# Kernel tuning notes

Hardware: AMD Instinct MI355X
Metric: run time of the kernel (lower is better)

## Reference

```python
import jax, jax.numpy as jnp
import numpy as np
import math

HEADS = 16
LAYER, NUM_LAYERS = 6, 12
ALPHA = 1.0 - math.tanh(math.pi * LAYER / NUM_LAYERS)
EPS = 1e-5


def _rot_half(t):
    d = t.shape[-1] // 2
    return jnp.concatenate([-t[..., d:], t[..., :d]], axis=-1)


def axial_rope(t):
    # t: [b, n, H, W, d]. Axial rotary: height rotates first d/2, width rotates second d/2.
    H, W, d = t.shape[2], t.shape[3], t.shape[4]
    half = d // 2
    inv_freq = 1.0 / (10000.0 ** (jnp.arange(0, half, 2, dtype=jnp.float32) / half))  # [half/2]
    ang_h = jnp.arange(H, dtype=jnp.float32)[:, None] * inv_freq[None, :]  # [H, half/2]
    ang_w = jnp.arange(W, dtype=jnp.float32)[:, None] * inv_freq[None, :]  # [W, half/2]
    ang_h = jnp.concatenate([ang_h, ang_h], axis=-1)  # [H, half]
    ang_w = jnp.concatenate([ang_w, ang_w], axis=-1)  # [W, half]
    ch, sh = jnp.cos(ang_h)[:, None, :], jnp.sin(ang_h)[:, None, :]  # [H,1,half]
    cw, sw = jnp.cos(ang_w)[None, :, :], jnp.sin(ang_w)[None, :, :]  # [1,W,half]
    th, tw = t[..., :half], t[..., half:]
    th = th * ch + _rot_half(th) * sh
    tw = tw * cw + _rot_half(tw) * sw
    return jnp.concatenate([th, tw], axis=-1)


def setup_inputs() -> dict:
    key = jax.random.key(0)
    ks = jax.random.split(key, 4)
    b, H, W, hid = 32, 28, 28, 1024
    return {
        "x": jax.random.normal(ks[0], (b, H, W, hid), jnp.float32),
        "input_img": jax.random.normal(ks[1], (b, H, W, hid), jnp.float32),
        "qkv_w": jax.random.normal(ks[2], (hid, 3 * hid), jnp.float32) * 0.02,
        "o_w": jax.random.normal(ks[3], (hid, hid), jnp.float32) * 0.02,
        "gn_w": jnp.ones((HEADS,), jnp.float32),
        "gn_b": jnp.zeros((HEADS,), jnp.float32),
    }


def reference(x, input_img, qkv_w, o_w, gn_w, gn_b):
    b, H, W, hid = x.shape
    n, dh = HEADS, hid // HEADS
    qkv = x @ qkv_w  # [b,H,W,3*hid]
    # 'b h w (c d) -> c b h w d'
    qkv = qkv.reshape(b, H, W, 3, hid).transpose(3, 0, 1, 2, 4)
    qkv = qkv + input_img[None] * ALPHA
    # 'c b h w (n d) -> c b n h w d'; unpack order is q, v, k
    qkv = qkv.reshape(3, b, H, W, n, dh).transpose(0, 1, 4, 2, 3, 5)
    q, v, k = qkv[0], qkv[1], qkv[2]
    gamma = (1.0 - 2.0 ** (-5.0 - jnp.arange(n, dtype=jnp.float32)))[None, :, None, None, None]
    k = k * gamma
    q, k = axial_rope(q), axial_rope(k)
    # attention along the W axis per row: [b,n,H,W,W]
    scores = jnp.einsum('bnhxd,bnhzd->bnhxz', q, k)
    # original einsum sums v over heights h as well as over y
    vsum = v.sum(axis=2)  # [b,n,W,dh]
    out = jnp.einsum('bnxwy,bnyd->bnxwd', scores, vsum)  # [b,n,H,W,dh]
    # GroupNorm(num_heads, num_heads): normalize each head over (H,W,dh)
    mu = out.mean(axis=(2, 3, 4), keepdims=True)
    var = out.var(axis=(2, 3, 4), keepdims=True)
    out = (out - mu) / jnp.sqrt(var + EPS)
    out = out * gn_w[None, :, None, None, None] + gn_b[None, :, None, None, None]
    # 'b n h w d -> b h w (n d)'
    out = out.transpose(0, 2, 3, 1, 4).reshape(b, H, W, hid)
    return out @ o_w
```

## Files before the change

kernel.cpp:

```cpp
#include <hip/hip_runtime.h>
#include <cstdint>
#include <cstddef>

#define HEADS 16
#define DH 64
#define BH 28
#define BWW 28
#define BATCH 32
#define HID 1024
#define M_ROWS 25088
#define ALPHA_C 0.082847664332725576f
#define EPS_C 1e-5f

typedef unsigned short ushort_t;
typedef __attribute__((ext_vector_type(8))) short bf16x8;
typedef __attribute__((ext_vector_type(4))) float f32x4;

__device__ inline unsigned short f2bf(float f) {
  unsigned int u = __builtin_bit_cast(unsigned int, f);
  u = (u + 0x7fffu + ((u >> 16) & 1u)) >> 16;
  return (unsigned short)u;
}
__device__ inline float bf2f(unsigned short h) {
  unsigned int u = ((unsigned int)h) << 16;
  return __builtin_bit_cast(float, u);
}

__global__ __launch_bounds__(256) void detect_k(const ushort_t* __restrict__ x,
                                                const ushort_t* __restrict__ qw,
                                                int* __restrict__ flagp) {
  int tid = threadIdx.x;
  int big = 0;
  #pragma unroll
  for (int j = 0; j < 4; ++j) {
    float a = fabsf(bf2f(x[tid * 4 + j]));
    float b = fabsf(bf2f(qw[tid * 4 + j]));
    if (!(a < 1e3f)) big++;
    if (!(b < 1e3f)) big++;
  }
  __shared__ int cnt;
  if (tid == 0) cnt = 0;
  __syncthreads();
  if (big) atomicAdd(&cnt, big);
  __syncthreads();
  if (tid == 0) *flagp = (cnt == 0) ? 1 : 0;
}

__global__ __launch_bounds__(256) void conv_x_k(const void* __restrict__ src,
                                                const int* __restrict__ flagp,
                                                ushort_t* __restrict__ dst, long n8) {
  if (*flagp) return;
  long i = (long)blockIdx.x * 256 + threadIdx.x;
  if (i >= n8) return;
  long e = i * 8;
  const float* sf = (const float*)src;
  float4 a = *(const float4*)(sf + e);
  float4 b = *(const float4*)(sf + e + 4);
  union { ushort_t u[8]; uint4 v; } o;
  o.u[0] = f2bf(a.x); o.u[1] = f2bf(a.y); o.u[2] = f2bf(a.z); o.u[3] = f2bf(a.w);
  o.u[4] = f2bf(b.x); o.u[5] = f2bf(b.y); o.u[6] = f2bf(b.z); o.u[7] = f2bf(b.w);
  *(uint4*)(dst + e) = o.v;
}

__global__ __launch_bounds__(256) void sumh_k(const void* __restrict__ x,
                                              const void* __restrict__ img,
                                              const int* __restrict__ flagp,
                                              ushort_t* __restrict__ xsum,
                                              float* __restrict__ imgsum) {
  int i = blockIdx.x * 256 + threadIdx.x;
  int c = i & 1023;
  int bw = i >> 10;
  int b = bw / BWW, w = bw % BWW;
  size_t base = ((size_t)b * BH * BWW + w) * HID + c;
  const size_t hstride = (size_t)BWW * HID;
  float sx = 0.f, si = 0.f;
  if (*flagp) {
    const ushort_t* xb = (const ushort_t*)x;
    const ushort_t* ib = (const ushort_t*)img;
    #pragma unroll 4
    for (int h = 0; h < BH; ++h) {
      sx += bf2f(xb[base + h * hstride]);
      si += bf2f(ib[base + h * hstride]);
    }
  } else {
    const float* xf = (const float*)x;
    const float* iff = (const float*)img;
    #pragma unroll 4
    for (int h = 0; h < BH; ++h) {
      sx += xf[base + h * hstride];
      si += iff[base + h * hstride];
    }
  }
  xsum[i] = f2bf(sx);
  imgsum[i] = si * ALPHA_C;
}

__global__ void transpose_any_k(const void* __restrict__ src, const int* __restrict__ flagp,
                                ushort_t* __restrict__ dst, int R, int C) {
  __shared__ float tile[32][33];
  int isbf = *flagp;
  int c0 = blockIdx.x * 32, r0 = blockIdx.y * 32;
  int tx = threadIdx.x, ty = threadIdx.y;
  const ushort_t* sb = (const ushort_t*)src;
  const float* sf = (const float*)src;
  #pragma unroll
  for (int i = ty; i < 32; i += 8) {
    size_t idx = (size_t)(r0 + i) * C + (c0 + tx);
    tile[i][tx] = isbf ? bf2f(sb[idx]) : sf[idx];
  }
  __syncthreads();
  #pragma unroll
  for (int i = ty; i < 32; i += 8)
    dst[(size_t)(c0 + i) * R + (r0 + tx)] = f2bf(tile[tx][i]);
}

#define BK 32

__global__ __launch_bounds__(256) void gemm_qkv_k(const void* __restrict__ x_raw,
                                                  const ushort_t* __restrict__ x_bf,
                                                  const ushort_t* __restrict__ Bt,
                                                  const void* __restrict__ img,
                                                  const int* __restrict__ flagp,
                                                  ushort_t* __restrict__ qbuf,
                                                  ushort_t* __restrict__ kbuf) {
  __shared__ ushort_t As[128 * BK];
  __shared__ ushort_t Bs[128 * BK];
  const int tid = threadIdx.x;
  const int K = 1024;
  const int ntile = 16;
  const int nt = blockIdx.x % ntile;
  const int n0 = (nt < 8) ? nt * 128 : nt * 128 + 1024;
  const int m0 = (blockIdx.x / ntile) * 128;
  const int lane = tid & 63;
  const int wave = tid >> 6;
  const int wm = (wave >> 1) * 64;
  const int wn = (wave & 1) * 64;
  const int fr = lane & 15;
  const int fq = lane >> 4;
  const int isbf = *flagp;
  const ushort_t* A = isbf ? (const ushort_t*)x_raw : x_bf;

  f32x4 acc[4][4] = {};
  const int srow = tid >> 2;
  const int skk  = (tid & 3) * 8;

  for (int k0 = 0; k0 < K; k0 += BK) {
    __syncthreads();
    const ushort_t* a0 = A + (size_t)(m0 + srow) * K + k0 + skk;
    const ushort_t* b0 = Bt + (size_t)(n0 + srow) * K + k0 + skk;
    __builtin_amdgcn_global_load_lds((const __attribute__((address_space(1))) unsigned int*)a0,
        (__attribute__((address_space(3))) unsigned int*)(As + tid * 8), 16, 0, 0);
    __builtin_amdgcn_global_load_lds((const __attribute__((address_space(1))) unsigned int*)(a0 + (size_t)64 * K),
        (__attribute__((address_space(3))) unsigned int*)(As + 2048 + tid * 8), 16, 0, 0);
    __builtin_amdgcn_global_load_lds((const __attribute__((address_space(1))) unsigned int*)b0,
        (__attribute__((address_space(3))) unsigned int*)(Bs + tid * 8), 16, 0, 0);
    __builtin_amdgcn_global_load_lds((const __attribute__((address_space(1))) unsigned int*)(b0 + (size_t)64 * K),
        (__attribute__((address_space(3))) unsigned int*)(Bs + 2048 + tid * 8), 16, 0, 0);
    __syncthreads();

    bf16x8 af[4], bfv[4];
    #pragma unroll
    for (int i = 0; i < 4; ++i)
      af[i] = *reinterpret_cast<const bf16x8*>(&As[(wm + i * 16 + fr) * BK + fq * 8]);
    #pragma unroll
    for (int i = 0; i < 4; ++i)
      bfv[i] = *reinterpret_cast<const bf16x8*>(&Bs[(wn + i * 16 + fr) * BK + fq * 8]);
    #pragma unroll
    for (int mi = 0; mi < 4; ++mi)
      #pragma unroll
      for (int ni = 0; ni < 4; ++ni)
        acc[mi][ni] = __builtin_amdgcn_mfma_f32_16x16x32_bf16(af[mi], bfv[ni], acc[mi][ni], 0, 0, 0);
  }

  const int colg = n0 + wn;
  const int t = colg >> 10;
  const int n = (colg & 1023) >> 6;
  const float gamma = 1.0f - exp2f(-5.0f - (float)n);
  const float invf = powf(10000.0f, -(float)fr / 16.0f);
  const ushort_t* imgb = (const ushort_t*)img;
  const float* imgf = (const float*)img;

  #pragma unroll
  for (int mi = 0; mi < 4; ++mi) {
    #pragma unroll
    for (int r = 0; r < 4; ++r) {
      int m = m0 + wm + mi * 16 + fq * 4 + r;
      int b = m / 784, rem = m % 784;
      int h = rem / 28, w = rem % 28;
      size_t ibase = (size_t)m * HID + n * DH + fr;
      float v0 = acc[mi][0][r] + (isbf ? bf2f(imgb[ibase])      : imgf[ibase])      * ALPHA_C;
      float v1 = acc[mi][1][r] + (isbf ? bf2f(imgb[ibase + 16]) : imgf[ibase + 16]) * ALPHA_C;
      float v2 = acc[mi][2][r] + (isbf ? bf2f(imgb[ibase + 32]) : imgf[ibase + 32]) * ALPHA_C;
      float v3 = acc[mi][3][r] + (isbf ? bf2f(imgb[ibase + 48]) : imgf[ibase + 48]) * ALPHA_C;
      if (t == 2) { v0 *= gamma; v1 *= gamma; v2 *= gamma; v3 *= gamma; }
      float snh, csh, snw, csw;
      __sincosf((float)h * invf, &snh, &csh);
      __sincosf((float)w * invf, &snw, &csw);
      float o0 = v0 * csh - v1 * snh;
      float o1 = v1 * csh + v0 * snh;
      float o2 = v2 * csw - v3 * snw;
      float o3 = v3 * csw + v2 * snw;
      ushort_t* dst = (t == 0 ? qbuf : kbuf) +
          (((((size_t)b * HEADS + n) * BH + h) * BWW + w) * DH) + fr;
      dst[0]  = f2bf(o0);
      dst[16] = f2bf(o1);
      dst[32] = f2bf(o2);
      dst[48] = f2bf(o3);
    }
  }
}

__global__ __launch_bounds__(256) void vsum_gemm_k(const ushort_t* __restrict__ A,
                                                   const ushort_t* __restrict__ Bt,
                                                   const float* __restrict__ imgsum,
                                                   float* __restrict__ vsum) {
  __shared__ ushort_t As[128 * BK];
  __shared__ ushort_t Bs[128 * BK];
  const int tid = threadIdx.x;
  const int K = 1024;
  const int n0 = (blockIdx.x % 8) * 128;
  const int m0 = (blockIdx.x / 8) * 128;
  const int lane = tid & 63;
  const int wave = tid >> 6;
  const int wm = (wave >> 1) * 64;
  const int wn = (wave & 1) * 64;
  const int fr = lane & 15;
  const int fq = lane >> 4;

  f32x4 acc[4][4] = {};
  const int srow = tid >> 2;
  const int skk  = (tid & 3) * 8;

  for (int k0 = 0; k0 < K; k0 += BK) {
    __syncthreads();
    const ushort_t* a0 = A + (size_t)(m0 + srow) * K + k0 + skk;
    const ushort_t* b0 = Bt + (size_t)(n0 + srow) * K + k0 + skk;
    __builtin_amdgcn_global_load_lds((const __attribute__((address_space(1))) unsigned int*)a0,
        (__attribute__((address_space(3))) unsigned int*)(As + tid * 8), 16, 0, 0);
    __builtin_amdgcn_global_load_lds((const __attribute__((address_space(1))) unsigned int*)(a0 + (size_t)64 * K),
        (__attribute__((address_space(3))) unsigned int*)(As + 2048 + tid * 8), 16, 0, 0);
    __builtin_amdgcn_global_load_lds((const __attribute__((address_space(1))) unsigned int*)b0,
        (__attribute__((address_space(3))) unsigned int*)(Bs + tid * 8), 16, 0, 0);
    __builtin_amdgcn_global_load_lds((const __attribute__((address_space(1))) unsigned int*)(b0 + (size_t)64 * K),
        (__attribute__((address_space(3))) unsigned int*)(Bs + 2048 + tid * 8), 16, 0, 0);
    __syncthreads();

    bf16x8 af[4], bfv[4];
    #pragma unroll
    for (int i = 0; i < 4; ++i)
      af[i] = *reinterpret_cast<const bf16x8*>(&As[(wm + i * 16 + fr) * BK + fq * 8]);
    #pragma unroll
    for (int i = 0; i < 4; ++i)
      bfv[i] = *reinterpret_cast<const bf16x8*>(&Bs[(wn + i * 16 + fr) * BK + fq * 8]);
    #pragma unroll
    for (int mi = 0; mi < 4; ++mi)
      #pragma unroll
      for (int ni = 0; ni < 4; ++ni)
        acc[mi][ni] = __builtin_amdgcn_mfma_f32_16x16x32_bf16(af[mi], bfv[ni], acc[mi][ni], 0, 0, 0);
  }

  #pragma unroll
  for (int mi = 0; mi < 4; ++mi)
    #pragma unroll
    for (int r = 0; r < 4; ++r) {
      int m = m0 + wm + mi * 16 + fq * 4 + r;
      int b = m / BWW, w = m % BWW;
      #pragma unroll
      for (int ni = 0; ni < 4; ++ni) {
        int col = n0 + wn + ni * 16 + fr;
        int n = col >> 6, d = col & 63;
        vsum[((((size_t)b * HEADS + n) * BWW) + w) * DH + d] =
            acc[mi][ni][r] + imgsum[(size_t)m * HID + col];
      }
    }
}

__global__ __launch_bounds__(256) void attn_k(const ushort_t* __restrict__ qbuf,
                                              const ushort_t* __restrict__ kbuf,
                                              const float* __restrict__ vsum,
                                              const void* __restrict__ gn_w,
                                              const void* __restrict__ gn_b,
                                              const int* __restrict__ flagp,
                                              ushort_t* __restrict__ xo) {
  __shared__ __align__(16) ushort_t outL[BH * BWW * DH];
  __shared__ ushort_t Vt[64 * 32];
  __shared__ ushort_t Sa[4][32 * 32];
  __shared__ float rs[4][2];
  __shared__ float mu_s, rstd_s;
  const int bn = blockIdx.x;
  const int b = bn >> 4, n = bn & 15;
  const int tid = threadIdx.x;
  const int lane = tid & 63, wv = tid >> 6;
  const int fr = lane & 15, fq = lane >> 4;
  const size_t vbase = (size_t)bn * BWW * DH;

  for (int e = tid; e < 64 * 32; e += 256) {
    int d = e >> 5, y = e & 31;
    Vt[e] = (y < BWW) ? f2bf(vsum[vbase + (size_t)y * DH + d]) : (ushort_t)0;
  }
  __syncthreads();

  bf16x8 bv[4];
  #pragma unroll
  for (int i = 0; i < 4; ++i)
    bv[i] = *reinterpret_cast<const bf16x8*>(&Vt[(i * 16 + fr) * 32 + fq * 8]);

  float lsum = 0.f, lsq = 0.f;
  ushort_t* sa = Sa[wv];

  for (int hi = 0; hi < 7; ++hi) {
    const int h = wv + hi * 4;
    const size_t qb = ((size_t)bn * BH + h) * BWW * DH;

    f32x4 s[2][2] = {};
    #pragma unroll
    for (int kk = 0; kk < 2; ++kk) {
      bf16x8 qf[2], kf[2];
      #pragma unroll
      for (int t = 0; t < 2; ++t) {
        qf[t] = *reinterpret_cast<const bf16x8*>(qbuf + qb + (size_t)(t * 16 + fr) * DH + kk * 32 + fq * 8);
        kf[t] = *reinterpret_cast<const bf16x8*>(kbuf + qb + (size_t)(t * 16 + fr) * DH + kk * 32 + fq * 8);
      }
      #pragma unroll
      for (int mt = 0; mt < 2; ++mt)
        #pragma unroll
        for (int nt = 0; nt < 2; ++nt)
          s[mt][nt] = __builtin_amdgcn_mfma_f32_16x16x32_bf16(qf[mt], kf[nt], s[mt][nt], 0, 0, 0);
    }

    #pragma unroll
    for (int mt = 0; mt < 2; ++mt)
      #pragma unroll
      for (int nt = 0; nt < 2; ++nt)
        #pragma unroll
        for (int r = 0; r < 4; ++r)
          sa[(mt * 16 + fq * 4 + r) * 32 + nt * 16 + fr] = f2bf(s[mt][nt][r]);
    __syncthreads();

    f32x4 o[2][4] = {};
    #pragma unroll
    for (int mt = 0; mt < 2; ++mt) {
      bf16x8 af = *reinterpret_cast<const bf16x8*>(&sa[(mt * 16 + fr) * 32 + fq * 8]);
      #pragma unroll
      for (int nt = 0; nt < 4; ++nt)
        o[mt][nt] = __builtin_amdgcn_mfma_f32_16x16x32_bf16(af, bv[nt], o[mt][nt], 0, 0, 0);
    }

    #pragma unroll
    for (int mt = 0; mt < 2; ++mt)
      #pragma unroll
      for (int r = 0; r < 4; ++r) {
        int w_ = mt * 16 + fq * 4 + r;
        if (w_ < BWW) {
          ushort_t* dl = outL + ((size_t)(h * BWW + w_) * DH) + fr;
          #pragma unroll
          for (int nt = 0; nt < 4; ++nt) {
            float v = o[mt][nt][r];
            dl[nt * 16] = f2bf(v);
            lsum += v; lsq += v * v;
          }
        }
      }
  }

  #pragma unroll
  for (int off = 32; off > 0; off >>= 1) {
    lsum += __shfl_down(lsum, off);
    lsq  += __shfl_down(lsq, off);
  }
  if (lane == 0) { rs[wv][0] = lsum; rs[wv][1] = lsq; }
  __syncthreads();
  if (tid == 0) {
    float s  = rs[0][0] + rs[1][0] + rs[2][0] + rs[3][0];
    float q2 = rs[0][1] + rs[1][1] + rs[2][1] + rs[3][1];
    const float Ninv = 1.0f / (float)(BH * BWW * DH);
    float mu = s * Ninv;
    float var = q2 * Ninv - mu * mu;
    mu_s = mu;
    rstd_s = rsqrtf(var + EPS_C);
  }
  __syncthreads();

  const int isbf = *flagp;
  const float gw = isbf ? bf2f(((const ushort_t*)gn_w)[n]) : ((const float*)gn_w)[n];
  const float gb = isbf ? bf2f(((const ushort_t*)gn_b)[n]) : ((const float*)gn_b)[n];
  const float sc = rstd_s * gw;
  const float sh_ = gb - mu_s * sc;
  for (int c = tid; c < BH * BWW * 8; c += 256) {
    int d8 = c & 7;
    int hw = c >> 3;
    int w = hw % BWW, h = hw / BWW;
    bf16x8 vv = *reinterpret_cast<const bf16x8*>(outL + (size_t)hw * DH + d8 * 8);
    union { ushort_t u[8]; uint4 q4; } o;
    #pragma unroll
    for (int j = 0; j < 8; ++j)
      o.u[j] = f2bf(bf2f((ushort_t)vv[j]) * sc + sh_);
    *(uint4*)(xo + (((size_t)(b * BH + h) * BWW + w) * HID) + n * DH + d8 * 8) = o.q4;
  }
}

__global__ __launch_bounds__(256) void gemm_bt_k(const ushort_t* __restrict__ A,
                                                 const ushort_t* __restrict__ Bt,
                                                 void* __restrict__ Cv,
                                                 const int* __restrict__ flagp,
                                                 int M, int N, int K) {
  __shared__ ushort_t As[128 * BK];
  __shared__ ushort_t Bs[128 * BK];
  const int tid = threadIdx.x;
  const int ntile = N / 128;
  const int n0 = (blockIdx.x % ntile) * 128;
  const int m0 = (blockIdx.x / ntile) * 128;
  const int lane = tid & 63;
  const int wave = tid >> 6;
  const int wm = (wave >> 1) * 64;
  const int wn = (wave & 1) * 64;
  const int fr = lane & 15;
  const int fq = lane >> 4;

  f32x4 acc[4][4] = {};
  const int srow = tid >> 2;
  const int skk  = (tid & 3) * 8;

  for (int k0 = 0; k0 < K; k0 += BK) {
    __syncthreads();
    const ushort_t* a0 = A + (size_t)(m0 + srow) * K + k0 + skk;
    const ushort_t* b0 = Bt + (size_t)(n0 + srow) * K + k0 + skk;
    __builtin_amdgcn_global_load_lds((const __attribute__((address_space(1))) unsigned int*)a0,
        (__attribute__((address_space(3))) unsigned int*)(As + tid * 8), 16, 0, 0);
    __builtin_amdgcn_global_load_lds((const __attribute__((address_space(1))) unsigned int*)(a0 + (size_t)64 * K),
        (__attribute__((address_space(3))) unsigned int*)(As + 2048 + tid * 8), 16, 0, 0);
    __builtin_amdgcn_global_load_lds((const __attribute__((address_space(1))) unsigned int*)b0,
        (__attribute__((address_space(3))) unsigned int*)(Bs + tid * 8), 16, 0, 0);
    __builtin_amdgcn_global_load_lds((const __attribute__((address_space(1))) unsigned int*)(b0 + (size_t)64 * K),
        (__attribute__((address_space(3))) unsigned int*)(Bs + 2048 + tid * 8), 16, 0, 0);
    __syncthreads();

    bf16x8 af[4], bfv[4];
    #pragma unroll
    for (int i = 0; i < 4; ++i)
      af[i] = *reinterpret_cast<const bf16x8*>(&As[(wm + i * 16 + fr) * BK + fq * 8]);
    #pragma unroll
    for (int i = 0; i < 4; ++i)
      bfv[i] = *reinterpret_cast<const bf16x8*>(&Bs[(wn + i * 16 + fr) * BK + fq * 8]);
    #pragma unroll
    for (int mi = 0; mi < 4; ++mi)
      #pragma unroll
      for (int ni = 0; ni < 4; ++ni)
        acc[mi][ni] = __builtin_amdgcn_mfma_f32_16x16x32_bf16(af[mi], bfv[ni], acc[mi][ni], 0, 0, 0);
  }

  int isbf = *flagp;
  if (isbf) {
    ushort_t* C = (ushort_t*)Cv;
    #pragma unroll
    for (int mi = 0; mi < 4; ++mi)
      #pragma unroll
      for (int r = 0; r < 4; ++r) {
        int m = m0 + wm + mi * 16 + fq * 4 + r;
        ushort_t* crow = C + (size_t)m * N + n0 + wn + fr;
        #pragma unroll
        for (int ni = 0; ni < 4; ++ni) crow[ni * 16] = f2bf(acc[mi][ni][r]);
      }
  } else {
    float* C = (float*)Cv;
    #pragma unroll
    for (int mi = 0; mi < 4; ++mi)
      #pragma unroll
      for (int r = 0; r < 4; ++r) {
        int m = m0 + wm + mi * 16 + fq * 4 + r;
        float* crow = C + (size_t)m * N + n0 + wn + fr;
        #pragma unroll
        for (int ni = 0; ni < 4; ++ni) crow[ni * 16] = acc[mi][ni][r];
      }
  }
}

extern "C" void kernel_launch(void* const* d_in, const int* in_sizes, int n_in,
                              void* d_out, int out_size, void* d_ws, size_t ws_size,
                              hipStream_t stream) {
  const void* x     = d_in[0];
  const void* img   = d_in[1];
  const void* qkv_w = d_in[2];
  const void* o_w   = d_in[3];
  const void* gn_w  = d_in[4];
  const void* gn_b  = d_in[5];

  char* ws = (char*)d_ws;
  ushort_t* x_bf   = (ushort_t*)(ws);
  ushort_t* xo     = (ushort_t*)(ws);
  ushort_t* qbuf   = (ushort_t*)(ws + 51380224);
  ushort_t* kbuf   = (ushort_t*)(ws + 102760448);
  float*    vsum   = (float*)(ws + 154140672);
  ushort_t* xsum   = (ushort_t*)(ws + 157810688);
  float*    imgsum = (float*)(ws + 159645696);
  int*      flag   = (int*)(ws + 163315712);
  ushort_t* w1T    = (ushort_t*)(ws + 163315968);
  ushort_t* w2T    = (ushort_t*)(ws + 169607424);

  detect_k<<<1, 256, 0, stream>>>((const ushort_t*)x, (const ushort_t*)qkv_w, flag);
  conv_x_k<<<12544, 256, 0, stream>>>(x, flag, x_bf, 3211264L);
  sumh_k<<<3584, 256, 0, stream>>>(x, img, flag, xsum, imgsum);
  transpose_any_k<<<dim3(96, 32), dim3(32, 8), 0, stream>>>(qkv_w, flag, w1T, 1024, 3072);
  transpose_any_k<<<dim3(32, 32), dim3(32, 8), 0, stream>>>(o_w, flag, w2T, 1024, 1024);

  gemm_qkv_k<<<196 * 16, 256, 0, stream>>>(x, x_bf, w1T, img, flag, qbuf, kbuf);
  vsum_gemm_k<<<56, 256, 0, stream>>>(xsum, w1T + (size_t)1024 * 1024, imgsum, vsum);

  attn_k<<<BATCH * HEADS, 256, 0, stream>>>(qbuf, kbuf, vsum, gn_w, gn_b, flag, xo);
  gemm_bt_k<<<196 * 8, 256, 0, stream>>>(xo, w2T, d_out, flag, M_ROWS, 1024, 1024);
}
```

Baseline: 637.6 us.

## Double-buffer LDS tiles in GEMMs and pre-convert input_img to bf16

All three MFMA GEMM kernels now use two LDS buffers, so the next K-tile is fetched with global_load_lds while the current tile feeds the MFMAs, and each iteration has one barrier instead of two. When inputs are fp32, input_img is also converted to bf16 in a separate pass, so the QKV epilogue reads 2-byte values instead of 4-byte ones. Workspace is reorganised so xsum/imgsum share qbuf's space, which requires running vsum_gemm before gemm_qkv. The cost is doubled LDS per block, which may reduce occupancy, plus an extra full-size conversion pass over input_img.

```diff
diff --git a/kernel.cpp b/kernel.cpp
--- a/kernel.cpp
+++ b/kernel.cpp
@@ -116,15 +116,29 @@
 
 #define BK 32
 
+#define STAGE(bufA, bufB, kk0) do {                                                              \
+  const ushort_t* a0_ = aRow + (kk0);                                                            \
+  const ushort_t* b0_ = bRow + (kk0);                                                            \
+  __builtin_amdgcn_global_load_lds((const __attribute__((address_space(1))) unsigned int*)a0_,   \
+      (__attribute__((address_space(3))) unsigned int*)((bufA) + tid * 8), 16, 0, 0);            \
+  __builtin_amdgcn_global_load_lds((const __attribute__((address_space(1))) unsigned int*)(a0_ + (size_t)64 * K), \
+      (__attribute__((address_space(3))) unsigned int*)((bufA) + 2048 + tid * 8), 16, 0, 0);     \
+  __builtin_amdgcn_global_load_lds((const __attribute__((address_space(1))) unsigned int*)b0_,   \
+      (__attribute__((address_space(3))) unsigned int*)((bufB) + tid * 8), 16, 0, 0);            \
+  __builtin_amdgcn_global_load_lds((const __attribute__((address_space(1))) unsigned int*)(b0_ + (size_t)64 * K), \
+      (__attribute__((address_space(3))) unsigned int*)((bufB) + 2048 + tid * 8), 16, 0, 0);     \
+} while (0)
+
 __global__ __launch_bounds__(256) void gemm_qkv_k(const void* __restrict__ x_raw,
                                                   const ushort_t* __restrict__ x_bf,
                                                   const ushort_t* __restrict__ Bt,
-                                                  const void* __restrict__ img,
+                                                  const void* __restrict__ img_raw,
+                                                  const ushort_t* __restrict__ img_bf,
                                                   const int* __restrict__ flagp,
                                                   ushort_t* __restrict__ qbuf,
                                                   ushort_t* __restrict__ kbuf) {
-  __shared__ ushort_t As[128 * BK];
-  __shared__ ushort_t Bs[128 * BK];
+  __shared__ ushort_t As[2][128 * BK];
+  __shared__ ushort_t Bs[2][128 * BK];
   const int tid = threadIdx.x;
   const int K = 1024;
   const int ntile = 16;
@@ -138,38 +152,35 @@
   const int fr = lane & 15;
   const int fq = lane >> 4;
   const int isbf = *flagp;
-  const ushort_t* A = isbf ? (const ushort_t*)x_raw : x_bf;
+  const ushort_t* A  = isbf ? (const ushort_t*)x_raw  : x_bf;
+  const ushort_t* IM = isbf ? (const ushort_t*)img_raw : img_bf;
 
   f32x4 acc[4][4] = {};
   const int srow = tid >> 2;
   const int skk  = (tid & 3) * 8;
-
+  const ushort_t* aRow = A  + (size_t)(m0 + srow) * K + skk;
+  const ushort_t* bRow = Bt + (size_t)(n0 + srow) * K + skk;
+
+  STAGE(As[0], Bs[0], 0);
+  __syncthreads();
+  int cur = 0;
   for (int k0 = 0; k0 < K; k0 += BK) {
-    __syncthreads();
-    const ushort_t* a0 = A + (size_t)(m0 + srow) * K + k0 + skk;
-    const ushort_t* b0 = Bt + (size_t)(n0 + srow) * K + k0 + skk;
-    __builtin_amdgcn_global_load_lds((const __attribute__((address_space(1))) unsigned int*)a0,
-        (__attribute__((address_space(3))) unsigned int*)(As + tid * 8), 16, 0, 0);
-    __builtin_amdgcn_global_load_lds((const __attribute__((address_space(1))) unsigned int*)(a0 + (size_t)64 * K),
-        (__attribute__((address_space(3))) unsigned int*)(As + 2048 + tid * 8), 16, 0, 0);
-    __builtin_amdgcn_global_load_lds((const __attribute__((address_space(1))) unsigned int*)b0,
-        (__attribute__((address_space(3))) unsigned int*)(Bs + tid * 8), 16, 0, 0);
-    __builtin_amdgcn_global_load_lds((const __attribute__((address_space(1))) unsigned int*)(b0 + (size_t)64 * K),
-        (__attribute__((address_space(3))) unsigned int*)(Bs + 2048 + tid * 8), 16, 0, 0);
-    __syncthreads();
-
+    int nxt = cur ^ 1;
+    if (k0 + BK < K) STAGE(As[nxt], Bs[nxt], k0 + BK);
     bf16x8 af[4], bfv[4];
     #pragma unroll
     for (int i = 0; i < 4; ++i)
-      af[i] = *reinterpret_cast<const bf16x8*>(&As[(wm + i * 16 + fr) * BK + fq * 8]);
+      af[i] = *reinterpret_cast<const bf16x8*>(&As[cur][(wm + i * 16 + fr) * BK + fq * 8]);
     #pragma unroll
     for (int i = 0; i < 4; ++i)
-      bfv[i] = *reinterpret_cast<const bf16x8*>(&Bs[(wn + i * 16 + fr) * BK + fq * 8]);
+      bfv[i] = *reinterpret_cast<const bf16x8*>(&Bs[cur][(wn + i * 16 + fr) * BK + fq * 8]);
     #pragma unroll
     for (int mi = 0; mi < 4; ++mi)
       #pragma unroll
       for (int ni = 0; ni < 4; ++ni)
         acc[mi][ni] = __builtin_amdgcn_mfma_f32_16x16x32_bf16(af[mi], bfv[ni], acc[mi][ni], 0, 0, 0);
+    __syncthreads();
+    cur = nxt;
   }
 
   const int colg = n0 + wn;
@@ -177,8 +188,6 @@
   const int n = (colg & 1023) >> 6;
   const float gamma = 1.0f - exp2f(-5.0f - (float)n);
   const float invf = powf(10000.0f, -(float)fr / 16.0f);
-  const ushort_t* imgb = (const ushort_t*)img;
-  const float* imgf = (const float*)img;
 
   #pragma unroll
   for (int mi = 0; mi < 4; ++mi) {
@@ -188,10 +197,10 @@
       int b = m / 784, rem = m % 784;
       int h = rem / 28, w = rem % 28;
       size_t ibase = (size_t)m * HID + n * DH + fr;
-      float v0 = acc[mi][0][r] + (isbf ? bf2f(imgb[ibase])      : imgf[ibase])      * ALPHA_C;
-      float v1 = acc[mi][1][r] + (isbf ? bf2f(imgb[ibase + 16]) : imgf[ibase + 16]) * ALPHA_C;
-      float v2 = acc[mi][2][r] + (isbf ? bf2f(imgb[ibase + 32]) : imgf[ibase + 32]) * ALPHA_C;
-      float v3 = acc[mi][3][r] + (isbf ? bf2f(imgb[ibase + 48]) : imgf[ibase + 48]) * ALPHA_C;
+      float v0 = acc[mi][0][r] + bf2f(IM[ibase])      * ALPHA_C;
+      float v1 = acc[mi][1][r] + bf2f(IM[ibase + 16]) * ALPHA_C;
+      float v2 = acc[mi][2][r] + bf2f(IM[ibase + 32]) * ALPHA_C;
+      float v3 = acc[mi][3][r] + bf2f(IM[ibase + 48]) * ALPHA_C;
       if (t == 2) { v0 *= gamma; v1 *= gamma; v2 *= gamma; v3 *= gamma; }
       float snh, csh, snw, csw;
       __sincosf((float)h * invf, &snh, &csh);
@@ -214,8 +223,8 @@
                                                    const ushort_t* __restrict__ Bt,
                                                    const float* __restrict__ imgsum,
                                                    float* __restrict__ vsum) {
-  __shared__ ushort_t As[128 * BK];
-  __shared__ ushort_t Bs[128 * BK];
+  __shared__ ushort_t As[2][128 * BK];
+  __shared__ ushort_t Bs[2][128 * BK];
   const int tid = threadIdx.x;
   const int K = 1024;
   const int n0 = (blockIdx.x % 8) * 128;
@@ -230,33 +239,29 @@
   f32x4 acc[4][4] = {};
   const int srow = tid >> 2;
   const int skk  = (tid & 3) * 8;
-
+  const ushort_t* aRow = A  + (size_t)(m0 + srow) * K + skk;
+  const ushort_t* bRow = Bt + (size_t)(n0 + srow) * K + skk;
+
+  STAGE(As[0], Bs[0], 0);
+  __syncthreads();
+  int cur = 0;
   for (int k0 = 0; k0 < K; k0 += BK) {
-    __syncthreads();
-    const ushort_t* a0 = A + (size_t)(m0 + srow) * K + k0 + skk;
-    const ushort_t* b0 = Bt + (size_t)(n0 + srow) * K + k0 + skk;
-    __builtin_amdgcn_global_load_lds((const __attribute__((address_space(1))) unsigned int*)a0,
-        (__attribute__((address_space(3))) unsigned int*)(As + tid * 8), 16, 0, 0);
-    __builtin_amdgcn_global_load_lds((const __attribute__((address_space(1))) unsigned int*)(a0 + (size_t)64 * K),
-        (__attribute__((address_space(3))) unsigned int*)(As + 2048 + tid * 8), 16, 0, 0);
-    __builtin_amdgcn_global_load_lds((const __attribute__((address_space(1))) unsigned int*)b0,
-        (__attribute__((address_space(3))) unsigned int*)(Bs + tid * 8), 16, 0, 0);
-    __builtin_amdgcn_global_load_lds((const __attribute__((address_space(1))) unsigned int*)(b0 + (size_t)64 * K),
-        (__attribute__((address_space(3))) unsigned int*)(Bs + 2048 + tid * 8), 16, 0, 0);
-    __syncthreads();
-
+    int nxt = cur ^ 1;
+    if (k0 + BK < K) STAGE(As[nxt], Bs[nxt], k0 + BK);
     bf16x8 af[4], bfv[4];
     #pragma unroll
     for (int i = 0; i < 4; ++i)
-      af[i] = *reinterpret_cast<const bf16x8*>(&As[(wm + i * 16 + fr) * BK + fq * 8]);
+      af[i] = *reinterpret_cast<const bf16x8*>(&As[cur][(wm + i * 16 + fr) * BK + fq * 8]);
     #pragma unroll
     for (int i = 0; i < 4; ++i)
-      bfv[i] = *reinterpret_cast<const bf16x8*>(&Bs[(wn + i * 16 + fr) * BK + fq * 8]);
+      bfv[i] = *reinterpret_cast<const bf16x8*>(&Bs[cur][(wn + i * 16 + fr) * BK + fq * 8]);
     #pragma unroll
     for (int mi = 0; mi < 4; ++mi)
       #pragma unroll
       for (int ni = 0; ni < 4; ++ni)
         acc[mi][ni] = __builtin_amdgcn_mfma_f32_16x16x32_bf16(af[mi], bfv[ni], acc[mi][ni], 0, 0, 0);
+    __syncthreads();
+    cur = nxt;
   }
 
   #pragma unroll
@@ -404,8 +409,8 @@
                                                  void* __restrict__ Cv,
                                                  const int* __restrict__ flagp,
                                                  int M, int N, int K) {
-  __shared__ ushort_t As[128 * BK];
-  __shared__ ushort_t Bs[128 * BK];
+  __shared__ ushort_t As[2][128 * BK];
+  __shared__ ushort_t Bs[2][128 * BK];
   const int tid = threadIdx.x;
   const int ntile = N / 128;
   const int n0 = (blockIdx.x % ntile) * 128;
@@ -420,33 +425,29 @@
   f32x4 acc[4][4] = {};
   const int srow = tid >> 2;
   const int skk  = (tid & 3) * 8;
-
+  const ushort_t* aRow = A  + (size_t)(m0 + srow) * K + skk;
+  const ushort_t* bRow = Bt + (size_t)(n0 + srow) * K + skk;
+
+  STAGE(As[0], Bs[0], 0);
+  __syncthreads();
+  int cur = 0;
   for (int k0 = 0; k0 < K; k0 += BK) {
-    __syncthreads();
-    const ushort_t* a0 = A + (size_t)(m0 + srow) * K + k0 + skk;
-    const ushort_t* b0 = Bt + (size_t)(n0 + srow) * K + k0 + skk;
-    __builtin_amdgcn_global_load_lds((const __attribute__((address_space(1))) unsigned int*)a0,
-        (__attribute__((address_space(3))) unsigned int*)(As + tid * 8), 16, 0, 0);
-    __builtin_amdgcn_global_load_lds((const __attribute__((address_space(1))) unsigned int*)(a0 + (size_t)64 * K),
-        (__attribute__((address_space(3))) unsigned int*)(As + 2048 + tid * 8), 16, 0, 0);
-    __builtin_amdgcn_global_load_lds((const __attribute__((address_space(1))) unsigned int*)b0,
-        (__attribute__((address_space(3))) unsigned int*)(Bs + tid * 8), 16, 0, 0);
-    __builtin_amdgcn_global_load_lds((const __attribute__((address_space(1))) unsigned int*)(b0 + (size_t)64 * K),
-        (__attribute__((address_space(3))) unsigned int*)(Bs + 2048 + tid * 8), 16, 0, 0);
-    __syncthreads();
-
+    int nxt = cur ^ 1;
+    if (k0 + BK < K) STAGE(As[nxt], Bs[nxt], k0 + BK);
     bf16x8 af[4], bfv[4];
     #pragma unroll
     for (int i = 0; i < 4; ++i)
-      af[i] = *reinterpret_cast<const bf16x8*>(&As[(wm + i * 16 + fr) * BK + fq * 8]);
+      af[i] = *reinterpret_cast<const bf16x8*>(&As[cur][(wm + i * 16 + fr) * BK + fq * 8]);
     #pragma unroll
     for (int i = 0; i < 4; ++i)
-      bfv[i] = *reinterpret_cast<const bf16x8*>(&Bs[(wn + i * 16 + fr) * BK + fq * 8]);
+      bfv[i] = *reinterpret_cast<const bf16x8*>(&Bs[cur][(wn + i * 16 + fr) * BK + fq * 8]);
     #pragma unroll
     for (int mi = 0; mi < 4; ++mi)
       #pragma unroll
       for (int ni = 0; ni < 4; ++ni)
         acc[mi][ni] = __builtin_amdgcn_mfma_f32_16x16x32_bf16(af[mi], bfv[ni], acc[mi][ni], 0, 0, 0);
+    __syncthreads();
+    cur = nxt;
   }
 
   int isbf = *flagp;
@@ -489,22 +490,24 @@
   ushort_t* x_bf   = (ushort_t*)(ws);
   ushort_t* xo     = (ushort_t*)(ws);
   ushort_t* qbuf   = (ushort_t*)(ws + 51380224);
+  ushort_t* xsum   = (ushort_t*)(ws + 51380224);
+  float*    imgsum = (float*)(ws + 53215232);
   ushort_t* kbuf   = (ushort_t*)(ws + 102760448);
   float*    vsum   = (float*)(ws + 154140672);
-  ushort_t* xsum   = (ushort_t*)(ws + 157810688);
-  float*    imgsum = (float*)(ws + 159645696);
-  int*      flag   = (int*)(ws + 163315712);
-  ushort_t* w1T    = (ushort_t*)(ws + 163315968);
-  ushort_t* w2T    = (ushort_t*)(ws + 169607424);
+  int*      flag   = (int*)(ws + 157810688);
+  ushort_t* w1T    = (ushort_t*)(ws + 157810944);
+  ushort_t* w2T    = (ushort_t*)(ws + 164102400);
+  ushort_t* img_bf = (ushort_t*)(ws + 166199552);
 
   detect_k<<<1, 256, 0, stream>>>((const ushort_t*)x, (const ushort_t*)qkv_w, flag);
-  conv_x_k<<<12544, 256, 0, stream>>>(x, flag, x_bf, 3211264L);
+  conv_x_k<<<12544, 256, 0, stream>>>(x,   flag, x_bf,   3211264L);
+  conv_x_k<<<12544, 256, 0, stream>>>(img, flag, img_bf, 3211264L);
   sumh_k<<<3584, 256, 0, stream>>>(x, img, flag, xsum, imgsum);
   transpose_any_k<<<dim3(96, 32), dim3(32, 8), 0, stream>>>(qkv_w, flag, w1T, 1024, 3072);
   transpose_any_k<<<dim3(32, 32), dim3(32, 8), 0, stream>>>(o_w, flag, w2T, 1024, 1024);
 
-  gemm_qkv_k<<<196 * 16, 256, 0, stream>>>(x, x_bf, w1T, img, flag, qbuf, kbuf);
   vsum_gemm_k<<<56, 256, 0, stream>>>(xsum, w1T + (size_t)1024 * 1024, imgsum, vsum);
+  gemm_qkv_k<<<196 * 16, 256, 0, stream>>>(x, x_bf, w1T, img, img_bf, flag, qbuf, kbuf);
 
   attn_k<<<BATCH * HEADS, 256, 0, stream>>>(qbuf, kbuf, vsum, gn_w, gn_b, flag, xo);
   gemm_bt_k<<<196 * 8, 256, 0, stream>>>(xo, w2T, d_out, flag, M_ROWS, 1024, 1024);
```

New measurement: 692.0 us. +8.5%, slower.
